# Kernel tuning notes

Measured on AMD Instinct MI355X. Metric: run time of the kernel, lower is better.

## Reference

```python
import jax, jax.numpy as jnp
import numpy as np

N = 50000      # nodes
E = 800000     # edges (before self-loops)
IN = 64        # in_dim
C = 64         # hidden_dim (per-head out channels)
H = 4          # heads
NEG_SLOPE = 0.2


def setup_inputs() -> dict:
    key = jax.random.key(0)
    ks = jax.random.split(key, 9)
    x = jax.random.normal(ks[0], (N, IN), jnp.float32)
    edge_index = jax.random.randint(ks[1], (2, E), 0, N)
    edge_attr = jax.random.uniform(ks[2], (E, 1), jnp.float32)
    s_in = 1.0 / np.sqrt(IN)
    s_c = 1.0 / np.sqrt(C)
    W = jax.random.normal(ks[3], (IN, H * C), jnp.float32) * s_in
    att_src = jax.random.normal(ks[4], (H, C), jnp.float32) * s_c
    att_dst = jax.random.normal(ks[5], (H, C), jnp.float32) * s_c
    lin_edge_w = jax.random.normal(ks[6], (1, H * C), jnp.float32)
    att_edge = jax.random.normal(ks[7], (H, C), jnp.float32) * s_c
    bias = jnp.zeros((C,), jnp.float32)
    return dict(x=x, edge_index=edge_index, edge_attr=edge_attr, W=W,
                att_src=att_src, att_dst=att_dst, lin_edge_w=lin_edge_w,
                att_edge=att_edge, bias=bias)


def reference(x, edge_index, edge_attr, W, att_src, att_dst, lin_edge_w, att_edge, bias):
    n = x.shape[0]
    # add self-loops (PyG default add_self_loops=True, fill_value='mean')
    loop = jnp.arange(n)
    src = jnp.concatenate([edge_index[0], loop])          # [E+N]
    dst = jnp.concatenate([edge_index[1], loop])          # [E+N]
    ea = jnp.concatenate([edge_attr,
                          jnp.full((n, 1), edge_attr.mean(), edge_attr.dtype)], axis=0)
    # node transform: [N, H, C]
    h = (x @ W).reshape(n, H, C)
    a_src = jnp.einsum('nhc,hc->nh', h, att_src)          # [N, H]
    a_dst = jnp.einsum('nhc,hc->nh', h, att_dst)          # [N, H]
    eh = (ea @ lin_edge_w).reshape(-1, H, C)              # [E+N, H, C]
    a_edge = jnp.einsum('ehc,hc->eh', eh, att_edge)       # [E+N, H]
    # per-edge attention logit
    alpha = a_src[src] + a_dst[dst] + a_edge              # [E+N, H]
    alpha = jax.nn.leaky_relu(alpha, NEG_SLOPE)
    # segment softmax over edges grouped by destination node
    amax = jax.ops.segment_max(alpha, dst, num_segments=n)
    alpha = jnp.exp(alpha - amax[dst])
    asum = jax.ops.segment_sum(alpha, dst, num_segments=n)
    alpha = alpha / (asum[dst] + 1e-16)                   # [E+N, H]
    # weighted message + scatter-add aggregation
    msg = h[src] * alpha[..., None]                       # [E+N, H, C]
    out = jax.ops.segment_sum(msg, dst, num_segments=n)   # [N, H, C]
    out = out.mean(axis=1) + bias                         # concat=False -> head mean
    # ReLU + residual
    return jax.nn.relu(out) + x
```

## Files before the change

kernel.cpp:

```cpp
#include <hip/hip_runtime.h>
#include <hip/hip_fp16.h>
#include <math.h>

#define H 4
#define C 64
#define HC 256
#define NEG 0.2f
#define MAXDEG 64
#define XPAD 72
#define HPAD 264

typedef __attribute__((ext_vector_type(8))) _Float16 half8;
typedef __attribute__((ext_vector_type(4))) float f32x4;
typedef float f32x2 __attribute__((vector_size(8)));

__global__ __launch_bounds__(256) void phase1_kernel(
    const float* __restrict__ x, const float* __restrict__ W,
    const float* __restrict__ att_src, const float* __restrict__ att_dst,
    const int* __restrict__ ei, const float* __restrict__ edge_attr,
    unsigned char* __restrict__ h, float* __restrict__ a_src, float* __restrict__ a_dst,
    unsigned* __restrict__ counts, unsigned* __restrict__ edges,
    float* __restrict__ mean_acc, int Nn, int Ee, int G1, int G2) {
    int t = threadIdx.x;
    if ((int)blockIdx.x < G1) {
        __shared__ __align__(16) _Float16 xs[16 * XPAD];
        __shared__ __align__(16) _Float16 hs[16 * HPAD];
        int w = t >> 6, lane = t & 63, quad = lane >> 4, c16 = lane & 15;
        half8 bf[4][2];
#pragma unroll
        for (int nt = 0; nt < 4; ++nt)
#pragma unroll
            for (int kh = 0; kh < 2; ++kh)
#pragma unroll
                for (int j = 0; j < 8; ++j)
                    bf[nt][kh][j] = (_Float16)W[(kh * 32 + quad * 8 + j) * HC +
                                                w * 64 + nt * 16 + c16];
        float ats[4], atd[4];
#pragma unroll
        for (int nt = 0; nt < 4; ++nt) {
            ats[nt] = att_src[w * 64 + nt * 16 + c16];
            atd[nt] = att_dst[w * 64 + nt * 16 + c16];
        }

        int nTiles = (Nn + 15) >> 4;
        for (int mt = blockIdx.x; mt < nTiles; mt += G1) {
            __syncthreads();
            {
                int row = t >> 4, col4 = (t & 15) * 4;
                int node = mt * 16 + row;
                float4 v = make_float4(0.f, 0.f, 0.f, 0.f);
                if (node < Nn) v = *(const float4*)(x + (size_t)node * 64 + col4);
                _Float16* dst = xs + row * XPAD + col4;
                dst[0] = (_Float16)v.x; dst[1] = (_Float16)v.y;
                dst[2] = (_Float16)v.z; dst[3] = (_Float16)v.w;
            }
            __syncthreads();
            half8 a0 = *(const half8*)(xs + c16 * XPAD + quad * 8);
            half8 a1 = *(const half8*)(xs + c16 * XPAD + 32 + quad * 8);
            f32x4 d[4];
#pragma unroll
            for (int nt = 0; nt < 4; ++nt) {
                f32x4 acc = {0.f, 0.f, 0.f, 0.f};
                acc = __builtin_amdgcn_mfma_f32_16x16x32_f16(a0, bf[nt][0], acc, 0, 0, 0);
                acc = __builtin_amdgcn_mfma_f32_16x16x32_f16(a1, bf[nt][1], acc, 0, 0, 0);
                d[nt] = acc;
            }
#pragma unroll
            for (int reg = 0; reg < 4; ++reg) {
                float ps = 0.f, pd = 0.f;
#pragma unroll
                for (int nt = 0; nt < 4; ++nt) {
                    ps += d[nt][reg] * ats[nt];
                    pd += d[nt][reg] * atd[nt];
                }
                ps += __shfl_xor(ps, 1); pd += __shfl_xor(pd, 1);
                ps += __shfl_xor(ps, 2); pd += __shfl_xor(pd, 2);
                ps += __shfl_xor(ps, 4); pd += __shfl_xor(pd, 4);
                ps += __shfl_xor(ps, 8); pd += __shfl_xor(pd, 8);
                if (c16 == 0) {
                    int node = mt * 16 + quad * 4 + reg;
                    if (node < Nn) {
                        a_src[node * 4 + w] = ps;
                        a_dst[node * 4 + w] = pd;
                    }
                }
            }
#pragma unroll
            for (int nt = 0; nt < 4; ++nt)
#pragma unroll
                for (int reg = 0; reg < 4; ++reg)
                    hs[(quad * 4 + reg) * HPAD + w * 64 + nt * 16 + c16] =
                        (_Float16)d[nt][reg];
            __syncthreads();
            {
                int row = t >> 4, chunk = t & 15;
                int node = mt * 16 + row;
                if (node < Nn) {
                    const uint4* sp = (const uint4*)(hs + row * HPAD + chunk * 16);
                    uint4 sA = sp[0], sB = sp[1];
                    unsigned ua[8] = {sA.x, sA.y, sA.z, sA.w, sB.x, sB.y, sB.z, sB.w};
                    unsigned ow[4];
#pragma unroll
                    for (int q = 0; q < 4; ++q) {
                        float2 p0 = __half22float2(*reinterpret_cast<const __half2*>(&ua[q * 2]));
                        float2 p1 = __half22float2(*reinterpret_cast<const __half2*>(&ua[q * 2 + 1]));
                        int v = __builtin_amdgcn_cvt_pk_fp8_f32(p0.x, p0.y, 0, false);
                        v = __builtin_amdgcn_cvt_pk_fp8_f32(p1.x, p1.y, v, true);
                        ow[q] = (unsigned)v;
                    }
                    *(uint4*)(h + (size_t)node * HC + chunk * 16) =
                        make_uint4(ow[0], ow[1], ow[2], ow[3]);
                }
            }
        }
    } else {
        __shared__ float red[256];
        int gid = ((int)blockIdx.x - G1) * 256 + t;
        int stride = G2 * 256;
        float s = 0.f;
        for (int i = gid; i < Ee; i += stride) {
            int src = ei[i];
            int dst = ei[Ee + i];
            float ea = edge_attr[i];
            s += ea;
            unsigned q = (unsigned)(ea * 65535.f + 0.5f);
            unsigned rank = atomicAdd(&counts[dst], 1u);
            if (rank < MAXDEG)
                edges[(size_t)dst * MAXDEG + rank] = (q << 16) | (unsigned)src;
        }
        red[t] = s;
        __syncthreads();
        for (int o = 128; o; o >>= 1) {
            if (t < o) red[t] += red[t + o];
            __syncthreads();
        }
        if (t == 0) atomicAdd(mean_acc, red[0]);
    }
}

__global__ __launch_bounds__(256) void aggregate_kernel(
    const unsigned* __restrict__ counts, const unsigned* __restrict__ edges,
    const float* __restrict__ a_src, const float* __restrict__ a_dst,
    const float* __restrict__ lin_edge_w, const float* __restrict__ att_edge,
    const float* __restrict__ mean_acc, const unsigned char* __restrict__ h,
    const float* __restrict__ bias, const float* __restrict__ x,
    float* __restrict__ out, int Nn, float invE) {
    int lane = threadIdx.x & 63;
    int n = blockIdx.x * 4 + (threadIdx.x >> 6);
    if (n >= Nn) return;
    int head = lane >> 4;

    int sub = lane & 15;
    float kp = 0.f;
#pragma unroll
    for (int j = 0; j < 4; ++j) {
        int c = sub * 4 + j;
        kp += lin_edge_w[head * C + c] * att_edge[head * C + c];
    }
    kp += __shfl_xor(kp, 1);
    kp += __shfl_xor(kp, 2);
    kp += __shfl_xor(kp, 4);
    kp += __shfl_xor(kp, 8);
    float K = kp;
    const float DEQ = 1.0f / 65535.f;

    float mean = mean_acc[0] * invE;
    unsigned deg = counts[n];
    if (deg > MAXDEG) deg = MAXDEG;
    size_t base = (size_t)n * MAXDEG;
    float ad = a_dst[n * 4 + head];
    const unsigned* h8 = (const unsigned*)h;

    float ls = a_src[n * 4 + head] + ad + mean * K;
    ls = ls > 0.f ? ls : NEG * ls;
    float wsl = __expf(ls);
    unsigned sv = h8[(size_t)n * 64 + lane];
    f32x2 s01 = __builtin_amdgcn_cvt_pk_f32_fp8((int)sv, false);
    f32x2 s23 = __builtin_amdgcn_cvt_pk_f32_fp8((int)sv, true);
    float4 acc = make_float4(wsl * s01[0], wsl * s01[1], wsl * s23[0], wsl * s23[1]);
    float swgt = wsl;

    int i = 0;
    for (; i + 4 <= (int)deg; i += 4) {
        unsigned r0 = edges[base + i + 0];
        unsigned r1 = edges[base + i + 1];
        unsigned r2 = edges[base + i + 2];
        unsigned r3 = edges[base + i + 3];
        int s0 = r0 & 0xFFFF, s1 = r1 & 0xFFFF, s2 = r2 & 0xFFFF, s3 = r3 & 0xFFFF;
        unsigned hv0 = h8[(size_t)s0 * 64 + lane];
        unsigned hv1 = h8[(size_t)s1 * 64 + lane];
        unsigned hv2 = h8[(size_t)s2 * 64 + lane];
        unsigned hv3 = h8[(size_t)s3 * 64 + lane];
        float l0 = a_src[s0 * 4 + head] + ad + (float)(r0 >> 16) * DEQ * K;
        float l1 = a_src[s1 * 4 + head] + ad + (float)(r1 >> 16) * DEQ * K;
        float l2 = a_src[s2 * 4 + head] + ad + (float)(r2 >> 16) * DEQ * K;
        float l3 = a_src[s3 * 4 + head] + ad + (float)(r3 >> 16) * DEQ * K;
        l0 = l0 > 0.f ? l0 : NEG * l0;
        l1 = l1 > 0.f ? l1 : NEG * l1;
        l2 = l2 > 0.f ? l2 : NEG * l2;
        l3 = l3 > 0.f ? l3 : NEG * l3;
        float w0 = __expf(l0), w1 = __expf(l1), w2 = __expf(l2), w3 = __expf(l3);
        swgt += (w0 + w1) + (w2 + w3);
        {
            f32x2 f01 = __builtin_amdgcn_cvt_pk_f32_fp8((int)hv0, false);
            f32x2 f23 = __builtin_amdgcn_cvt_pk_f32_fp8((int)hv0, true);
            acc.x += w0 * f01[0]; acc.y += w0 * f01[1];
            acc.z += w0 * f23[0]; acc.w += w0 * f23[1];
        }
        {
            f32x2 f01 = __builtin_amdgcn_cvt_pk_f32_fp8((int)hv1, false);
            f32x2 f23 = __builtin_amdgcn_cvt_pk_f32_fp8((int)hv1, true);
            acc.x += w1 * f01[0]; acc.y += w1 * f01[1];
            acc.z += w1 * f23[0]; acc.w += w1 * f23[1];
        }
        {
            f32x2 f01 = __builtin_amdgcn_cvt_pk_f32_fp8((int)hv2, false);
            f32x2 f23 = __builtin_amdgcn_cvt_pk_f32_fp8((int)hv2, true);
            acc.x += w2 * f01[0]; acc.y += w2 * f01[1];
            acc.z += w2 * f23[0]; acc.w += w2 * f23[1];
        }
        {
            f32x2 f01 = __builtin_amdgcn_cvt_pk_f32_fp8((int)hv3, false);
            f32x2 f23 = __builtin_amdgcn_cvt_pk_f32_fp8((int)hv3, true);
            acc.x += w3 * f01[0]; acc.y += w3 * f01[1];
            acc.z += w3 * f23[0]; acc.w += w3 * f23[1];
        }
    }
    for (; i < (int)deg; ++i) {
        unsigned r = edges[base + i];
        int s0 = r & 0xFFFF;
        unsigned hv = h8[(size_t)s0 * 64 + lane];
        float l = a_src[s0 * 4 + head] + ad + (float)(r >> 16) * DEQ * K;
        l = l > 0.f ? l : NEG * l;
        float wg = __expf(l);
        swgt += wg;
        f32x2 f01 = __builtin_amdgcn_cvt_pk_f32_fp8((int)hv, false);
        f32x2 f23 = __builtin_amdgcn_cvt_pk_f32_fp8((int)hv, true);
        acc.x += wg * f01[0]; acc.y += wg * f01[1];
        acc.z += wg * f23[0]; acc.w += wg * f23[1];
    }

    float inv = 1.f / (swgt + 1e-16f);
    acc.x *= inv; acc.y *= inv; acc.z *= inv; acc.w *= inv;

    acc.x += __shfl_xor(acc.x, 16);
    acc.y += __shfl_xor(acc.y, 16);
    acc.z += __shfl_xor(acc.z, 16);
    acc.w += __shfl_xor(acc.w, 16);
    acc.x += __shfl_xor(acc.x, 32);
    acc.y += __shfl_xor(acc.y, 32);
    acc.z += __shfl_xor(acc.z, 32);
    acc.w += __shfl_xor(acc.w, 32);
    if (lane < 16) {
        float4 b = ((const float4*)bias)[lane];
        float4 xv = ((const float4*)x)[(size_t)n * 16 + lane];
        float4 o;
        o.x = fmaxf(acc.x * 0.25f + b.x, 0.f) + xv.x;
        o.y = fmaxf(acc.y * 0.25f + b.y, 0.f) + xv.y;
        o.z = fmaxf(acc.z * 0.25f + b.z, 0.f) + xv.z;
        o.w = fmaxf(acc.w * 0.25f + b.w, 0.f) + xv.w;
        ((float4*)out)[(size_t)n * 16 + lane] = o;
    }
}

extern "C" void kernel_launch(void* const* d_in, const int* in_sizes, int n_in,
                              void* d_out, int out_size, void* d_ws, size_t ws_size,
                              hipStream_t stream) {
    const float* x = (const float*)d_in[0];
    const int* ei = (const int*)d_in[1];
    const float* edge_attr = (const float*)d_in[2];
    const float* W = (const float*)d_in[3];
    const float* att_src = (const float*)d_in[4];
    const float* att_dst = (const float*)d_in[5];
    const float* lin_edge_w = (const float*)d_in[6];
    const float* att_edge = (const float*)d_in[7];
    const float* bias = (const float*)d_in[8];
    float* out = (float*)d_out;
    int Nn = in_sizes[0] / 64;
    int Ee = in_sizes[1] / 2;

    char* p = (char*)d_ws;
    size_t off = 0;
    auto alloc = [&](size_t bytes) -> char* {
        char* r = p + off;
        off += (bytes + 255) & ~(size_t)255;
        return r;
    };
    float* mean_acc = (float*)alloc(256);
    unsigned* counts = (unsigned*)alloc((size_t)Nn * 4);
    size_t zero_bytes = off;
    unsigned* edges = (unsigned*)alloc((size_t)Nn * MAXDEG * 4);
    unsigned char* h = (unsigned char*)alloc((size_t)Nn * HC);
    float* a_src = (float*)alloc((size_t)Nn * H * 4);
    float* a_dst = (float*)alloc((size_t)Nn * H * 4);
    (void)ws_size;

    const int G1 = 512, G2 = 1536;
    hipMemsetAsync(d_ws, 0, zero_bytes, stream);
    phase1_kernel<<<G1 + G2, 256, 0, stream>>>(x, W, att_src, att_dst, ei, edge_attr,
                                               h, a_src, a_dst, counts, edges,
                                               mean_acc, Nn, Ee, G1, G2);
    aggregate_kernel<<<(Nn + 3) / 4, 256, 0, stream>>>(counts, edges, a_src, a_dst,
                                                       lin_edge_w, att_edge, mean_acc,
                                                       h, bias, x, out, Nn,
                                                       1.0f / (float)Ee);
}
```

Measured before the change: 177.2 us.

## Embed per-node edge count in row header and broadcast records via readlane

Stores each destination node's atomic counter as the first word of its edge-record row, removing the separate counts array. The aggregate kernel loads the whole row with one coalesced per-lane load and pulls records out with readlane instead of issuing serial loads inside the loop. The memset now has to zero the full edge table rather than just the counts, which adds write traffic. Per-node capacity drops to 63 records.

Result: faster. 170.0 us (-4.0%).

```diff
diff --git a/kernel.cpp b/kernel.cpp
--- a/kernel.cpp
+++ b/kernel.cpp
@@ -6,7 +6,8 @@
 #define C 64
 #define HC 256
 #define NEG 0.2f
-#define MAXDEG 64
+#define ROWU 64
+#define MAXREC 63
 #define XPAD 72
 #define HPAD 264
 
@@ -19,8 +20,8 @@
     const float* __restrict__ att_src, const float* __restrict__ att_dst,
     const int* __restrict__ ei, const float* __restrict__ edge_attr,
     unsigned char* __restrict__ h, float* __restrict__ a_src, float* __restrict__ a_dst,
-    unsigned* __restrict__ counts, unsigned* __restrict__ edges,
-    float* __restrict__ mean_acc, int Nn, int Ee, int G1, int G2) {
+    unsigned* __restrict__ edges, float* __restrict__ mean_acc,
+    int Nn, int Ee, int G1, int G2) {
     int t = threadIdx.x;
     if ((int)blockIdx.x < G1) {
         __shared__ __align__(16) _Float16 xs[16 * XPAD];
@@ -124,9 +125,9 @@
             float ea = edge_attr[i];
             s += ea;
             unsigned q = (unsigned)(ea * 65535.f + 0.5f);
-            unsigned rank = atomicAdd(&counts[dst], 1u);
-            if (rank < MAXDEG)
-                edges[(size_t)dst * MAXDEG + rank] = (q << 16) | (unsigned)src;
+            unsigned rank = atomicAdd(&edges[(size_t)dst * ROWU], 1u);
+            if (rank < MAXREC)
+                edges[(size_t)dst * ROWU + 1 + rank] = (q << 16) | (unsigned)src;
         }
         red[t] = s;
         __syncthreads();
@@ -139,7 +140,7 @@
 }
 
 __global__ __launch_bounds__(256) void aggregate_kernel(
-    const unsigned* __restrict__ counts, const unsigned* __restrict__ edges,
+    const unsigned* __restrict__ edges,
     const float* __restrict__ a_src, const float* __restrict__ a_dst,
     const float* __restrict__ lin_edge_w, const float* __restrict__ att_edge,
     const float* __restrict__ mean_acc, const unsigned char* __restrict__ h,
@@ -150,6 +151,15 @@
     if (n >= Nn) return;
     int head = lane >> 4;
 
+    size_t rowbase = (size_t)n * ROWU;
+    unsigned deg = edges[rowbase];
+    unsigned rec = edges[rowbase + 1 + lane];
+    const unsigned* h8 = (const unsigned*)h;
+    unsigned sv = h8[(size_t)n * 64 + lane];
+    float mean = mean_acc[0] * invE;
+    float ad = a_dst[n * 4 + head];
+    float asn = a_src[n * 4 + head];
+
     int sub = lane & 15;
     float kp = 0.f;
 #pragma unroll
@@ -164,17 +174,11 @@
     float K = kp;
     const float DEQ = 1.0f / 65535.f;
 
-    float mean = mean_acc[0] * invE;
-    unsigned deg = counts[n];
-    if (deg > MAXDEG) deg = MAXDEG;
-    size_t base = (size_t)n * MAXDEG;
-    float ad = a_dst[n * 4 + head];
-    const unsigned* h8 = (const unsigned*)h;
-
-    float ls = a_src[n * 4 + head] + ad + mean * K;
+    if (deg > MAXREC) deg = MAXREC;
+
+    float ls = asn + ad + mean * K;
     ls = ls > 0.f ? ls : NEG * ls;
     float wsl = __expf(ls);
-    unsigned sv = h8[(size_t)n * 64 + lane];
     f32x2 s01 = __builtin_amdgcn_cvt_pk_f32_fp8((int)sv, false);
     f32x2 s23 = __builtin_amdgcn_cvt_pk_f32_fp8((int)sv, true);
     float4 acc = make_float4(wsl * s01[0], wsl * s01[1], wsl * s23[0], wsl * s23[1]);
@@ -182,10 +186,10 @@
 
     int i = 0;
     for (; i + 4 <= (int)deg; i += 4) {
-        unsigned r0 = edges[base + i + 0];
-        unsigned r1 = edges[base + i + 1];
-        unsigned r2 = edges[base + i + 2];
-        unsigned r3 = edges[base + i + 3];
+        unsigned r0 = (unsigned)__builtin_amdgcn_readlane((int)rec, i + 0);
+        unsigned r1 = (unsigned)__builtin_amdgcn_readlane((int)rec, i + 1);
+        unsigned r2 = (unsigned)__builtin_amdgcn_readlane((int)rec, i + 2);
+        unsigned r3 = (unsigned)__builtin_amdgcn_readlane((int)rec, i + 3);
         int s0 = r0 & 0xFFFF, s1 = r1 & 0xFFFF, s2 = r2 & 0xFFFF, s3 = r3 & 0xFFFF;
         unsigned hv0 = h8[(size_t)s0 * 64 + lane];
         unsigned hv1 = h8[(size_t)s1 * 64 + lane];
@@ -227,7 +231,7 @@
         }
     }
     for (; i < (int)deg; ++i) {
-        unsigned r = edges[base + i];
+        unsigned r = (unsigned)__builtin_amdgcn_readlane((int)rec, i);
         int s0 = r & 0xFFFF;
         unsigned hv = h8[(size_t)s0 * 64 + lane];
         float l = a_src[s0 * 4 + head] + ad + (float)(r >> 16) * DEQ * K;
@@ -287,9 +291,8 @@
         return r;
     };
     float* mean_acc = (float*)alloc(256);
-    unsigned* counts = (unsigned*)alloc((size_t)Nn * 4);
+    unsigned* edges = (unsigned*)alloc((size_t)Nn * ROWU * 4);
     size_t zero_bytes = off;
-    unsigned* edges = (unsigned*)alloc((size_t)Nn * MAXDEG * 4);
     unsigned char* h = (unsigned char*)alloc((size_t)Nn * HC);
     float* a_src = (float*)alloc((size_t)Nn * H * 4);
     float* a_dst = (float*)alloc((size_t)Nn * H * 4);
@@ -298,9 +301,9 @@
     const int G1 = 512, G2 = 1536;
     hipMemsetAsync(d_ws, 0, zero_bytes, stream);
     phase1_kernel<<<G1 + G2, 256, 0, stream>>>(x, W, att_src, att_dst, ei, edge_attr,
-                                               h, a_src, a_dst, counts, edges,
+                                               h, a_src, a_dst, edges,
                                                mean_acc, Nn, Ee, G1, G2);
-    aggregate_kernel<<<(Nn + 3) / 4, 256, 0, stream>>>(counts, edges, a_src, a_dst,
+    aggregate_kernel<<<(Nn + 3) / 4, 256, 0, stream>>>(edges, a_src, a_dst,
                                                        lin_edge_w, att_edge, mean_acc,
                                                        h, bias, x, out, Nn,
                                                        1.0f / (float)Ee);
```
